# Optimization experiments

Measured on AMD Instinct MI355X. Metric: run time of the kernel, lower is better.

## Reference

```python
import jax, jax.numpy as jnp
import numpy as np

D = 64        # GatedGraphConv out_channels
N_LAYERS = 5  # number of stacked convs


def setup_inputs() -> dict:
    key = jax.random.key(0)
    ks = jax.random.split(key, 16)
    N, E, G = 100000, 1600000, 64
    s = 0.1
    inp = {
        'conv_weight': jax.random.normal(ks[0], (N_LAYERS, D, D), jnp.float32) * s,
        'gru_w_ih':    jax.random.normal(ks[1], (N_LAYERS, 3 * D, D), jnp.float32) * s,
        'gru_w_hh':    jax.random.normal(ks[2], (N_LAYERS, 3 * D, D), jnp.float32) * s,
        'gru_b_ih':    jax.random.normal(ks[3], (N_LAYERS, 3 * D), jnp.float32) * s,
        'gru_b_hh':    jax.random.normal(ks[4], (N_LAYERS, 3 * D), jnp.float32) * s,
        'fc1_w': jax.random.normal(ks[5], (32, D), jnp.float32) * s,
        'fc1_b': jax.random.normal(ks[6], (32,), jnp.float32) * s,
        'fc2_w': jax.random.normal(ks[7], (16, 32), jnp.float32) * s,
        'fc2_b': jax.random.normal(ks[8], (16,), jnp.float32) * s,
        'fc3_w': jax.random.normal(ks[9], (1, 16), jnp.float32) * s,
        'fc3_b': jax.random.normal(ks[10], (1,), jnp.float32) * s,
        'edge_index': jax.random.randint(ks[11], (2, E), 0, N, jnp.int64 if jax.config.jax_enable_x64 else jnp.int32),
        'batch': jnp.sort(jax.random.randint(ks[12], (N,), 0, G, jnp.int32)),
        'num_nodes': N,
        'num_graphs': G,
    }
    return inp


def _gru_cell(m, h, w_ih, w_hh, b_ih, b_hh):
    # torch.nn.GRUCell math; m: [N,D] input, h: [N,D] hidden
    gi = m @ w_ih.T + b_ih   # [N, 3D]
    gh = h @ w_hh.T + b_hh   # [N, 3D]
    i_r, i_z, i_n = jnp.split(gi, 3, axis=1)
    h_r, h_z, h_n = jnp.split(gh, 3, axis=1)
    r = jax.nn.sigmoid(i_r + h_r)
    z = jax.nn.sigmoid(i_z + h_z)
    n = jnp.tanh(i_n + r * h_n)
    return (1.0 - z) * n + z * h


def reference(conv_weight, gru_w_ih, gru_w_hh, gru_b_ih, gru_b_hh,
              fc1_w, fc1_b, fc2_w, fc2_b, fc3_w, fc3_b,
              edge_index, batch, num_nodes, num_graphs):
    src, dst = edge_index[0], edge_index[1]  # source_to_target flow
    # initial node features: zeros [N,8] zero-padded to D by GatedGraphConv
    x0 = jnp.zeros((num_nodes, D), jnp.float32)

    def step(x, params):
        w, wih, whh, bih, bhh = params
        m = x @ w                                        # [N, D]
        agg = jax.ops.segment_sum(m[src], dst, num_segments=num_nodes)  # scatter-add
        return _gru_cell(agg, x, wih, whh, bih, bhh), None

    x, _ = jax.lax.scan(step, x0,
                        (conv_weight, gru_w_ih, gru_w_hh, gru_b_ih, gru_b_hh))

    # scatter_add pooling over batch -> [num_graphs, D]
    g = jax.ops.segment_sum(x, batch, num_segments=num_graphs)
    h = jax.nn.elu(g @ fc1_w.T + fc1_b)
    h = jax.nn.elu(h @ fc2_w.T + fc2_b)
    return h @ fc3_w.T + fc3_b  # [num_graphs, 1]
```

## Files before the change

### kernel.cpp

```cpp
#include <hip/hip_runtime.h>
#include <math.h>

typedef _Float16 f16x2 __attribute__((ext_vector_type(2)));
typedef _Float16 f16x4 __attribute__((ext_vector_type(4)));
typedef _Float16 f16x8 __attribute__((ext_vector_type(8)));
typedef float f32x4 __attribute__((ext_vector_type(4)));

#define CBITS 10
#define FCHUNK 4096
#define MATSZ 13056
__device__ __forceinline__ int woff(int row) { return 64 * row + 8 * (row >> 1); }

__device__ __forceinline__ float sigmoidf_(float v) {
  return 1.0f / (1.0f + __expf(-v));
}
__device__ __forceinline__ float tanhf_(float v) {
  v = fminf(fmaxf(v, -15.f), 15.f);
  float e = __expf(2.f * v);
  return (e - 1.f) / (e + 1.f);
}
__device__ __forceinline__ float eluf_(float v) { return v > 0.f ? v : (__expf(v) - 1.f); }

__global__ __launch_bounds__(256) void fuse_w_kernel(const float* __restrict__ conv_w,
                                                     const float* __restrict__ w_ih,
                                                     _Float16* __restrict__ wcS) {
  const int l = blockIdx.x >> 2;
  const int j0 = (blockIdx.x & 3) * 48;
  const float* W = conv_w + (size_t)l * 4096;
  const float* wi = w_ih + (size_t)l * 12288;
  _Float16* out = wcS + (size_t)l * MATSZ;
  __shared__ float sWt[64 * 68];
  __shared__ float sI[48 * 64];
  const int t = threadIdx.x;
  for (int i = t; i < 4096; i += 256) sWt[(i & 63) * 68 + (i >> 6)] = W[i];
  for (int i = t; i < 3072; i += 256) sI[i] = wi[j0 * 64 + i];
  __syncthreads();
#pragma unroll
  for (int r = 0; r < 3; ++r) {
    int u = t + 256 * r;
    int j = u >> 4, cg = (u & 15) * 4;
    float4 a = {0.f, 0.f, 0.f, 0.f};
    for (int k = 0; k < 64; ++k) {
      float4 w = *(const float4*)(sWt + k * 68 + cg);
      float s = sI[j * 64 + k];
      a.x += w.x * s; a.y += w.y * s; a.z += w.z * s; a.w += w.w * s;
    }
    int row = j0 + j;
    f16x4 hv;
    hv[0] = (_Float16)a.x; hv[1] = (_Float16)a.y;
    hv[2] = (_Float16)a.z; hv[3] = (_Float16)a.w;
    *(f16x4*)(out + woff(row) + cg) = hv;
  }
}

__global__ __launch_bounds__(256) void whh_prep_kernel(const float* __restrict__ whh,
                                                       _Float16* __restrict__ whhS) {
  int idx = blockIdx.x * 256 + threadIdx.x;
  if (idx >= 15360) return;
  int l = idx / 3072, rem = idx % 3072;
  int r = rem >> 4, c4 = (rem & 15) * 4;
  float4 v = *(const float4*)(whh + (size_t)l * 12288 + r * 64 + c4);
  f16x4 hv;
  hv[0] = (_Float16)v.x; hv[1] = (_Float16)v.y;
  hv[2] = (_Float16)v.z; hv[3] = (_Float16)v.w;
  *(f16x4*)(whhS + (size_t)l * MATSZ + woff(r) + c4) = hv;
}

__global__ __launch_bounds__(256) void bucket_hist_kernel(const int* __restrict__ dst,
                                                          int* __restrict__ bh, int E) {
  __shared__ int h[128];
  const int t = threadIdx.x;
  if (t < 128) h[t] = 0;
  __syncthreads();
  for (int e = blockIdx.x * 256 + t; e < E; e += gridDim.x * 256)
    atomicAdd(&h[dst[e] >> CBITS], 1);
  __syncthreads();
  if (t < 128 && h[t]) atomicAdd(&bh[t * 16], h[t]);
}

__global__ __launch_bounds__(128) void bucket_scan_kernel(int* __restrict__ bh, int nbk,
                                                          int* __restrict__ boffs, int E) {
  __shared__ int s[128];
  const int t = threadIdx.x;
  int v = (t < nbk) ? bh[t * 16] : 0;
  s[t] = v;
  __syncthreads();
  for (int o = 1; o < 128; o <<= 1) {
    int a = (t >= o) ? s[t - o] : 0;
    __syncthreads();
    s[t] += a;
    __syncthreads();
  }
  if (t < nbk) {
    int ex = s[t] - v;
    boffs[t] = ex;
    bh[t * 16] = ex;
  }
  if (t == 0) boffs[nbk] = E;
}

__global__ __launch_bounds__(256) void bucket_fill_kernel(const int* __restrict__ src,
                                                          const int* __restrict__ dst,
                                                          int* __restrict__ bcur,
                                                          unsigned* __restrict__ pairs, int E) {
  __shared__ uint2 staged[FCHUNK];
  __shared__ int h[128], lbase[128], gbase[128], lcur[128];
  const int t = threadIdx.x;
  const int e0 = blockIdx.x * FCHUNK;
  int cnt = E - e0;
  if (cnt > FCHUNK) cnt = FCHUNK;
  if (t < 128) h[t] = 0;
  __syncthreads();
  for (int i = t; i < cnt; i += 256) atomicAdd(&h[dst[e0 + i] >> CBITS], 1);
  __syncthreads();
  if (t < 128) lcur[t] = h[t];
  __syncthreads();
  for (int o = 1; o < 128; o <<= 1) {
    int a = 0;
    if (t < 128 && t >= o) a = lcur[t - o];
    __syncthreads();
    if (t < 128) lcur[t] += a;
    __syncthreads();
  }
  if (t < 128) {
    int ex = lcur[t] - h[t];
    lbase[t] = ex;
    if (h[t]) gbase[t] = atomicAdd(&bcur[t * 16], h[t]);
    lcur[t] = ex;
  }
  __syncthreads();
  for (int i = t; i < cnt; i += 256) {
    int d = dst[e0 + i];
    int b = d >> CBITS;
    int p = atomicAdd(&lcur[b], 1);
    staged[p] = make_uint2((unsigned)src[e0 + i], (unsigned)d);
  }
  __syncthreads();
  for (int i = t; i < cnt; i += 256) {
    uint2 pr = staged[i];
    int b = (int)(pr.y >> CBITS);
    pairs[gbase[b] + (i - lbase[b])] = (pr.x << CBITS) | (pr.y & ((1u << CBITS) - 1));
  }
}

__global__ __launch_bounds__(256) void csr_build_kernel(const unsigned* __restrict__ pairs,
                                                        const int* __restrict__ boffs,
                                                        int* __restrict__ offs,
                                                        int* __restrict__ srcs, int N, int E) {
  const int b = blockIdx.x, t = threadIdx.x;
  const int nbase = b << CBITS;
  __shared__ int deg[1024];
  __shared__ int ssc[256];
  for (int i = t; i < 1024; i += 256) deg[i] = 0;
  __syncthreads();
  const int beg = boffs[b], end = boffs[b + 1];
  for (int e = beg + t; e < end; e += 256) atomicAdd(&deg[pairs[e] & 1023], 1);
  __syncthreads();
  int d0 = deg[4 * t], d1 = deg[4 * t + 1], d2 = deg[4 * t + 2], d3 = deg[4 * t + 3];
  int s = d0 + d1 + d2 + d3;
  ssc[t] = s;
  __syncthreads();
  for (int o = 1; o < 256; o <<= 1) {
    int a = (t >= o) ? ssc[t - o] : 0;
    __syncthreads();
    ssc[t] += a;
    __syncthreads();
  }
  int base = beg + ssc[t] - s;
  int c0 = base, c1 = c0 + d0, c2 = c1 + d1, c3 = c2 + d2;
  if (nbase + 4 * t + 0 < N) offs[nbase + 4 * t + 0] = c0;
  if (nbase + 4 * t + 1 < N) offs[nbase + 4 * t + 1] = c1;
  if (nbase + 4 * t + 2 < N) offs[nbase + 4 * t + 2] = c2;
  if (nbase + 4 * t + 3 < N) offs[nbase + 4 * t + 3] = c3;
  deg[4 * t] = c0; deg[4 * t + 1] = c1; deg[4 * t + 2] = c2; deg[4 * t + 3] = c3;
  if (b == 0 && t == 0) offs[N] = E;
  if (b == 0 && t < 64) srcs[E + t] = 0;
  __syncthreads();
  for (int e = beg + t; e < end; e += 256) {
    unsigned p = pairs[e];
    int pos = atomicAdd(&deg[p & 1023], 1);
    srcs[pos] = (int)(p >> CBITS);
  }
}

__global__ __launch_bounds__(64) void h1_kernel(const float* __restrict__ b_ih,
                                                const float* __restrict__ b_hh,
                                                float* __restrict__ h1) {
  int d = threadIdx.x;
  float r = sigmoidf_(b_ih[d] + b_hh[d]);
  float z = sigmoidf_(b_ih[64 + d] + b_hh[64 + d]);
  float n = tanhf_(b_ih[128 + d] + r * b_hh[128 + d]);
  h1[d] = (1.f - z) * n;
}

__global__ __launch_bounds__(256) void bcast_kernel(const int* __restrict__ offs,
                                                    const float* __restrict__ h1,
                                                    _Float16* __restrict__ xh,
                                                    _Float16* __restrict__ aggh,
                                                    int N, int units) {
  int idx = blockIdx.x * 256 + threadIdx.x;
  if (idx >= units) return;
  int v = idx >> 5, lp = idx & 31;
  float2 hh = *(const float2*)(h1 + lp * 2);
  f16x2 hv;
  hv[0] = (_Float16)hh.x; hv[1] = (_Float16)hh.y;
  *(f16x2*)(xh + (size_t)idx * 2) = hv;
  float dg = (v < N) ? (float)(offs[v + 1] - offs[v]) : 0.f;
  f16x2 av;
  av[0] = (_Float16)(dg * hh.x); av[1] = (_Float16)(dg * hh.y);
  *(f16x2*)(aggh + (size_t)idx * 2) = av;
}

__global__ __launch_bounds__(256) void agg_kernel(const _Float16* __restrict__ xh,
                                                  const int* __restrict__ offs,
                                                  const int* __restrict__ srcs,
                                                  _Float16* __restrict__ aggh, int N) {
  int wave = threadIdx.x >> 6, lane = threadIdx.x & 63;
  int v = blockIdx.x * 4 + wave;
  if (v >= N) return;
  const int beg = offs[v], end = offs[v + 1];
  const int deg = end - beg;
  const int og = lane >> 3;
  const int lp = lane & 7;
  f16x8 acc = {};
  for (int base = 0; base < deg; base += 64) {
    const int cnt = min(64, deg - base);
    int sidx = srcs[beg + base + lane];
    for (int e = 0; e < cnt; e += 8) {
      int me = e + og;
      int s = __shfl(sidx, me);
      f16x8 vv = *(const f16x8*)(xh + (size_t)s * 64 + lp * 8);
      if (me < cnt) acc += vv;
    }
  }
#pragma unroll
  for (int off = 8; off < 64; off <<= 1) {
    union { f16x8 h; int i[4]; } a, b;
    a.h = acc;
#pragma unroll
    for (int w = 0; w < 4; ++w) b.i[w] = __shfl_xor(a.i[w], off);
    acc += b.h;
  }
  if (og == 0) *(f16x8*)(aggh + (size_t)v * 64 + lp * 8) = acc;
}

__global__ __launch_bounds__(256) void gru_kernel(const _Float16* __restrict__ aggh,
                                                  _Float16* __restrict__ xh,
                                                  const _Float16* __restrict__ wcS,
                                                  const _Float16* __restrict__ whhS,
                                                  const float* __restrict__ b_ih,
                                                  const float* __restrict__ b_hh,
                                                  int N, int numTiles) {
  __shared__ _Float16 sW[2 * MATSZ];
  const int t = threadIdx.x;
  for (int i = t; i < 2 * (MATSZ / 8); i += 256) {
    int mat = (i >= MATSZ / 8);
    int idx = i - mat * (MATSZ / 8);
    *(f16x8*)(sW + mat * MATSZ + idx * 8) =
        *(const f16x8*)((mat ? whhS : wcS) + idx * 8);
  }
  __syncthreads();
  const int wave = t >> 6, lane = t & 63;
  const int q = lane >> 4, c = lane & 15;
  float bRZ[4], bZZ[4], bIN[4], bHN[4];
#pragma unroll
  for (int dt = 0; dt < 4; ++dt) {
    int d = dt * 16 + c;
    bRZ[dt] = b_ih[d] + b_hh[d];
    bZZ[dt] = b_ih[64 + d] + b_hh[64 + d];
    bIN[dt] = b_ih[128 + d];
    bHN[dt] = b_hh[128 + d];
  }
  f16x8 idf[4];
#pragma unroll
  for (int dt = 0; dt < 4; ++dt) {
    int tgt = (dt & 1) * 16 + c - q * 8;
#pragma unroll
    for (int j = 0; j < 8; ++j) idf[dt][j] = (j == tgt) ? (_Float16)1.0f : (_Float16)0.0f;
  }
  for (int tile = blockIdx.x; tile < numTiles; tile += gridDim.x) {
    const int nb0 = tile * 64 + wave * 16;
    const size_t rowbase = (size_t)(nb0 + c) * 64;
    f16x8 aA[2], aH[2];
#pragma unroll
    for (int ks = 0; ks < 2; ++ks) {
      aA[ks] = *(const f16x8*)(aggh + rowbase + ks * 32 + q * 8);
      aH[ks] = *(const f16x8*)(xh + rowbase + ks * 32 + q * 8);
    }
    f32x4 aR[4], aZ[4], aN[4], aHNa[4], aHO[4];
#pragma unroll
    for (int dt = 0; dt < 4; ++dt) {
      aR[dt] = (f32x4){bRZ[dt], bRZ[dt], bRZ[dt], bRZ[dt]};
      aZ[dt] = (f32x4){bZZ[dt], bZZ[dt], bZZ[dt], bZZ[dt]};
      aN[dt] = (f32x4){bIN[dt], bIN[dt], bIN[dt], bIN[dt]};
      aHNa[dt] = (f32x4){bHN[dt], bHN[dt], bHN[dt], bHN[dt]};
      aHO[dt] = (f32x4){0.f, 0.f, 0.f, 0.f};
    }
#pragma unroll
    for (int ks = 0; ks < 2; ++ks) {
      const int colo = ks * 32 + q * 8;
#pragma unroll
      for (int dt = 0; dt < 4; ++dt) {
        const int r0 = dt * 16 + c;
        f16x8 bWr = *(const f16x8*)(sW + woff(r0) + colo);
        f16x8 bHr = *(const f16x8*)(sW + MATSZ + woff(r0) + colo);
        f16x8 bWz = *(const f16x8*)(sW + woff(64 + r0) + colo);
        f16x8 bHz = *(const f16x8*)(sW + MATSZ + woff(64 + r0) + colo);
        f16x8 bWn = *(const f16x8*)(sW + woff(128 + r0) + colo);
        f16x8 bHn = *(const f16x8*)(sW + MATSZ + woff(128 + r0) + colo);
        aR[dt] = __builtin_amdgcn_mfma_f32_16x16x32_f16(aA[ks], bWr, aR[dt], 0, 0, 0);
        aR[dt] = __builtin_amdgcn_mfma_f32_16x16x32_f16(aH[ks], bHr, aR[dt], 0, 0, 0);
        aZ[dt] = __builtin_amdgcn_mfma_f32_16x16x32_f16(aA[ks], bWz, aZ[dt], 0, 0, 0);
        aZ[dt] = __builtin_amdgcn_mfma_f32_16x16x32_f16(aH[ks], bHz, aZ[dt], 0, 0, 0);
        aN[dt] = __builtin_amdgcn_mfma_f32_16x16x32_f16(aA[ks], bWn, aN[dt], 0, 0, 0);
        aHNa[dt] = __builtin_amdgcn_mfma_f32_16x16x32_f16(aH[ks], bHn, aHNa[dt], 0, 0, 0);
      }
    }
#pragma unroll
    for (int dt = 0; dt < 4; ++dt)
      aHO[dt] = __builtin_amdgcn_mfma_f32_16x16x32_f16(aH[dt >> 1], idf[dt], aHO[dt], 0, 0, 0);
#pragma unroll
    for (int dt = 0; dt < 4; ++dt) {
      int d = dt * 16 + c;
#pragma unroll
      for (int r = 0; r < 4; ++r) {
        int node = nb0 + q * 4 + r;
        if (node < N) {
          float rr = sigmoidf_(aR[dt][r]);
          float zz = sigmoidf_(aZ[dt][r]);
          float nn = tanhf_(aN[dt][r] + rr * aHNa[dt][r]);
          float out = nn + zz * (aHO[dt][r] - nn);
          xh[(size_t)node * 64 + d] = (_Float16)out;
        }
      }
    }
  }
}

__global__ __launch_bounds__(256) void pool_kernel(const _Float16* __restrict__ xh,
                                                   const int* __restrict__ batch,
                                                   float* __restrict__ g, int N) {
  int wave = threadIdx.x >> 6, lane = threadIdx.x & 63;
  int n0 = blockIdx.x * 64 + wave * 16;
  if (n0 >= N) return;
  int end = n0 + 16;
  if (end > N) end = N;
  int cur = batch[n0];
  float acc = 0.f;
  for (int n = n0; n < end; ++n) {
    int b = batch[n];
    if (b != cur) {
      atomicAdd(&g[(size_t)cur * 64 + lane], acc);
      acc = 0.f;
      cur = b;
    }
    acc += (float)xh[(size_t)n * 64 + lane];
  }
  atomicAdd(&g[(size_t)cur * 64 + lane], acc);
}

__global__ __launch_bounds__(256) void mlp_kernel(const float* __restrict__ g,
                                                  const float* __restrict__ w1,
                                                  const float* __restrict__ b1,
                                                  const float* __restrict__ w2,
                                                  const float* __restrict__ b2,
                                                  const float* __restrict__ w3,
                                                  const float* __restrict__ b3,
                                                  float* __restrict__ out, int G) {
  __shared__ float sG[64 * 64];
  __shared__ float sH1[64 * 32];
  __shared__ float sH2[64 * 16];
  int t = threadIdx.x;
  for (int i = t; i < G * 64; i += 256) sG[i] = g[i];
  __syncthreads();
  for (int o = t; o < G * 32; o += 256) {
    int gi = o >> 5, i = o & 31;
    float a = b1[i];
    for (int k = 0; k < 64; ++k) a += sG[gi * 64 + k] * w1[i * 64 + k];
    sH1[gi * 32 + i] = eluf_(a);
  }
  __syncthreads();
  for (int o = t; o < G * 16; o += 256) {
    int gi = o >> 4, i = o & 15;
    float a = b2[i];
    for (int k = 0; k < 32; ++k) a += sH1[gi * 32 + k] * w2[i * 32 + k];
    sH2[gi * 16 + i] = eluf_(a);
  }
  __syncthreads();
  for (int o = t; o < G; o += 256) {
    float a = b3[0];
    for (int k = 0; k < 16; ++k) a += sH2[o * 16 + k] * w3[k];
    out[o] = a;
  }
}

extern "C" void kernel_launch(void* const* d_in, const int* in_sizes, int n_in,
                              void* d_out, int out_size, void* d_ws, size_t ws_size,
                              hipStream_t stream) {
  const float* conv_w = (const float*)d_in[0];
  const float* w_ih = (const float*)d_in[1];
  const float* w_hh = (const float*)d_in[2];
  const float* b_ih = (const float*)d_in[3];
  const float* b_hh = (const float*)d_in[4];
  const float* fc1_w = (const float*)d_in[5];
  const float* fc1_b = (const float*)d_in[6];
  const float* fc2_w = (const float*)d_in[7];
  const float* fc2_b = (const float*)d_in[8];
  const float* fc3_w = (const float*)d_in[9];
  const float* fc3_b = (const float*)d_in[10];
  const int* ei = (const int*)d_in[11];
  const int* batch = (const int*)d_in[12];
  const int N = in_sizes[12];
  const int E = in_sizes[11] / 2;
  const int G = out_size;
  const int* src = ei;
  const int* dst = ei + E;
  const int nbk = (N + 1023) >> CBITS;
  const int tiles = (N + 63) / 64;
  const int Npad = tiles * 64;

  char* ws = (char*)d_ws;
  size_t off = 0;
  auto alloc = [&](size_t bytes) -> void* {
    void* p = ws + off;
    off += (bytes + 255) & ~(size_t)255;
    return p;
  };
  _Float16* xh = (_Float16*)alloc((size_t)Npad * 64 * 2);
  _Float16* aggh = (_Float16*)alloc((size_t)Npad * 64 * 2);
  _Float16* wcS = (_Float16*)alloc((size_t)5 * MATSZ * 2);
  _Float16* whhS = (_Float16*)alloc((size_t)5 * MATSZ * 2);
  float* h1 = (float*)alloc(64 * 4);
  float* gbuf = (float*)alloc((size_t)G * 64 * 4);
  int* offs = (int*)alloc((size_t)(N + 1) * 4);
  int* srcs = (int*)alloc((size_t)(E + 64) * 4);
  unsigned* pairs = (unsigned*)alloc((size_t)E * 4);
  int* bh = (int*)alloc(128 * 16 * 4);
  int* boffs = (int*)alloc(129 * 4);

  hipMemsetAsync(bh, 0, 128 * 16 * 4, stream);
  bucket_hist_kernel<<<256, 256, 0, stream>>>(dst, bh, E);
  bucket_scan_kernel<<<1, 128, 0, stream>>>(bh, nbk, boffs, E);
  bucket_fill_kernel<<<(E + FCHUNK - 1) / FCHUNK, 256, 0, stream>>>(src, dst, bh, pairs, E);
  csr_build_kernel<<<nbk, 256, 0, stream>>>(pairs, boffs, offs, srcs, N, E);

  fuse_w_kernel<<<20, 256, 0, stream>>>(conv_w, w_ih, wcS);
  whh_prep_kernel<<<60, 256, 0, stream>>>(w_hh, whhS);

  h1_kernel<<<1, 64, 0, stream>>>(b_ih, b_hh, h1);
  bcast_kernel<<<(Npad * 32 + 255) / 256, 256, 0, stream>>>(offs, h1, xh, aggh, N, Npad * 32);

  gru_kernel<<<768, 256, 0, stream>>>(aggh, xh, wcS + MATSZ, whhS + MATSZ,
                                      b_ih + 192, b_hh + 192, N, tiles);
  for (int l = 2; l < 5; ++l) {
    agg_kernel<<<(N + 3) / 4, 256, 0, stream>>>(xh, offs, srcs, aggh, N);
    gru_kernel<<<768, 256, 0, stream>>>(aggh, xh, wcS + (size_t)l * MATSZ,
                                        whhS + (size_t)l * MATSZ, b_ih + (size_t)l * 192,
                                        b_hh + (size_t)l * 192, N, tiles);
  }

  hipMemsetAsync(gbuf, 0, (size_t)G * 64 * 4, stream);
  pool_kernel<<<(N + 63) / 64, 256, 0, stream>>>(xh, batch, gbuf, N);
  mlp_kernel<<<1, 256, 0, stream>>>(gbuf, fc1_w, fc1_b, fc2_w, fc2_b, fc3_w, fc3_b,
                                    (float*)d_out, G);
}
```

Before: 448.0 us.

## Split GRU tiles into output-column halves with ping-pong hidden-state buffers

Each GRU work item now computes only half of the 64 output columns for a 64-node tile, which doubles the number of work items and halves the accumulator registers per wave. This should raise occupancy and spread the work across more parallel units. Because two work items now read the same node rows while writing different columns, the hidden state becomes double-buffered (separate input and output arrays) so an in-place write cannot corrupt another item's read. The cost is that the aggregated-message and hidden-state rows are loaded twice, and one extra buffer is allocated.

```diff
diff --git a/kernel.cpp b/kernel.cpp
--- a/kernel.cpp
+++ b/kernel.cpp
@@ -245,12 +245,13 @@
 }
 
 __global__ __launch_bounds__(256) void gru_kernel(const _Float16* __restrict__ aggh,
-                                                  _Float16* __restrict__ xh,
+                                                  const _Float16* __restrict__ xh_in,
+                                                  _Float16* __restrict__ xh_out,
                                                   const _Float16* __restrict__ wcS,
                                                   const _Float16* __restrict__ whhS,
                                                   const float* __restrict__ b_ih,
                                                   const float* __restrict__ b_hh,
-                                                  int N, int numTiles) {
+                                                  int N, int numIter) {
   __shared__ _Float16 sW[2 * MATSZ];
   const int t = threadIdx.x;
   for (int i = t; i < 2 * (MATSZ / 8); i += 256) {
@@ -271,66 +272,72 @@
     bIN[dt] = b_ih[128 + d];
     bHN[dt] = b_hh[128 + d];
   }
-  f16x8 idf[4];
-#pragma unroll
-  for (int dt = 0; dt < 4; ++dt) {
-    int tgt = (dt & 1) * 16 + c - q * 8;
-#pragma unroll
-    for (int j = 0; j < 8; ++j) idf[dt][j] = (j == tgt) ? (_Float16)1.0f : (_Float16)0.0f;
-  }
-  for (int tile = blockIdx.x; tile < numTiles; tile += gridDim.x) {
+  f16x8 idf[2];
+#pragma unroll
+  for (int p = 0; p < 2; ++p) {
+    int tgt = p * 16 + c - q * 8;
+#pragma unroll
+    for (int j = 0; j < 8; ++j) idf[p][j] = (j == tgt) ? (_Float16)1.0f : (_Float16)0.0f;
+  }
+#pragma unroll 1
+  for (int it = blockIdx.x; it < numIter; it += gridDim.x) {
+    const int tile = it >> 1, half = it & 1;
     const int nb0 = tile * 64 + wave * 16;
     const size_t rowbase = (size_t)(nb0 + c) * 64;
     f16x8 aA[2], aH[2];
 #pragma unroll
     for (int ks = 0; ks < 2; ++ks) {
       aA[ks] = *(const f16x8*)(aggh + rowbase + ks * 32 + q * 8);
-      aH[ks] = *(const f16x8*)(xh + rowbase + ks * 32 + q * 8);
-    }
-    f32x4 aR[4], aZ[4], aN[4], aHNa[4], aHO[4];
-#pragma unroll
-    for (int dt = 0; dt < 4; ++dt) {
-      aR[dt] = (f32x4){bRZ[dt], bRZ[dt], bRZ[dt], bRZ[dt]};
-      aZ[dt] = (f32x4){bZZ[dt], bZZ[dt], bZZ[dt], bZZ[dt]};
-      aN[dt] = (f32x4){bIN[dt], bIN[dt], bIN[dt], bIN[dt]};
-      aHNa[dt] = (f32x4){bHN[dt], bHN[dt], bHN[dt], bHN[dt]};
-      aHO[dt] = (f32x4){0.f, 0.f, 0.f, 0.f};
+      aH[ks] = *(const f16x8*)(xh_in + rowbase + ks * 32 + q * 8);
+    }
+    f32x4 aR[2], aZ[2], aN[2], aHNa[2], aHO[2];
+#pragma unroll
+    for (int p = 0; p < 2; ++p) {
+      float brz = half ? bRZ[2 + p] : bRZ[p];
+      float bzz = half ? bZZ[2 + p] : bZZ[p];
+      float bin = half ? bIN[2 + p] : bIN[p];
+      float bhn = half ? bHN[2 + p] : bHN[p];
+      aR[p] = (f32x4){brz, brz, brz, brz};
+      aZ[p] = (f32x4){bzz, bzz, bzz, bzz};
+      aN[p] = (f32x4){bin, bin, bin, bin};
+      aHNa[p] = (f32x4){bhn, bhn, bhn, bhn};
+      aHO[p] = (f32x4){0.f, 0.f, 0.f, 0.f};
     }
 #pragma unroll
     for (int ks = 0; ks < 2; ++ks) {
       const int colo = ks * 32 + q * 8;
 #pragma unroll
-      for (int dt = 0; dt < 4; ++dt) {
-        const int r0 = dt * 16 + c;
+      for (int p = 0; p < 2; ++p) {
+        const int r0 = (half * 2 + p) * 16 + c;
         f16x8 bWr = *(const f16x8*)(sW + woff(r0) + colo);
         f16x8 bHr = *(const f16x8*)(sW + MATSZ + woff(r0) + colo);
         f16x8 bWz = *(const f16x8*)(sW + woff(64 + r0) + colo);
         f16x8 bHz = *(const f16x8*)(sW + MATSZ + woff(64 + r0) + colo);
         f16x8 bWn = *(const f16x8*)(sW + woff(128 + r0) + colo);
         f16x8 bHn = *(const f16x8*)(sW + MATSZ + woff(128 + r0) + colo);
-        aR[dt] = __builtin_amdgcn_mfma_f32_16x16x32_f16(aA[ks], bWr, aR[dt], 0, 0, 0);
-        aR[dt] = __builtin_amdgcn_mfma_f32_16x16x32_f16(aH[ks], bHr, aR[dt], 0, 0, 0);
-        aZ[dt] = __builtin_amdgcn_mfma_f32_16x16x32_f16(aA[ks], bWz, aZ[dt], 0, 0, 0);
-        aZ[dt] = __builtin_amdgcn_mfma_f32_16x16x32_f16(aH[ks], bHz, aZ[dt], 0, 0, 0);
-        aN[dt] = __builtin_amdgcn_mfma_f32_16x16x32_f16(aA[ks], bWn, aN[dt], 0, 0, 0);
-        aHNa[dt] = __builtin_amdgcn_mfma_f32_16x16x32_f16(aH[ks], bHn, aHNa[dt], 0, 0, 0);
+        aR[p] = __builtin_amdgcn_mfma_f32_16x16x32_f16(aA[ks], bWr, aR[p], 0, 0, 0);
+        aR[p] = __builtin_amdgcn_mfma_f32_16x16x32_f16(aH[ks], bHr, aR[p], 0, 0, 0);
+        aZ[p] = __builtin_amdgcn_mfma_f32_16x16x32_f16(aA[ks], bWz, aZ[p], 0, 0, 0);
+        aZ[p] = __builtin_amdgcn_mfma_f32_16x16x32_f16(aH[ks], bHz, aZ[p], 0, 0, 0);
+        aN[p] = __builtin_amdgcn_mfma_f32_16x16x32_f16(aA[ks], bWn, aN[p], 0, 0, 0);
+        aHNa[p] = __builtin_amdgcn_mfma_f32_16x16x32_f16(aH[ks], bHn, aHNa[p], 0, 0, 0);
       }
     }
 #pragma unroll
-    for (int dt = 0; dt < 4; ++dt)
-      aHO[dt] = __builtin_amdgcn_mfma_f32_16x16x32_f16(aH[dt >> 1], idf[dt], aHO[dt], 0, 0, 0);
-#pragma unroll
-    for (int dt = 0; dt < 4; ++dt) {
-      int d = dt * 16 + c;
+    for (int p = 0; p < 2; ++p)
+      aHO[p] = __builtin_amdgcn_mfma_f32_16x16x32_f16(aH[half], idf[p], aHO[p], 0, 0, 0);
+#pragma unroll
+    for (int p = 0; p < 2; ++p) {
+      int d = (half * 2 + p) * 16 + c;
 #pragma unroll
       for (int r = 0; r < 4; ++r) {
         int node = nb0 + q * 4 + r;
         if (node < N) {
-          float rr = sigmoidf_(aR[dt][r]);
-          float zz = sigmoidf_(aZ[dt][r]);
-          float nn = tanhf_(aN[dt][r] + rr * aHNa[dt][r]);
-          float out = nn + zz * (aHO[dt][r] - nn);
-          xh[(size_t)node * 64 + d] = (_Float16)out;
+          float rr = sigmoidf_(aR[p][r]);
+          float zz = sigmoidf_(aZ[p][r]);
+          float nn = tanhf_(aN[p][r] + rr * aHNa[p][r]);
+          float out = nn + zz * (aHO[p][r] - nn);
+          xh_out[(size_t)node * 64 + d] = (_Float16)out;
         }
       }
     }
@@ -418,6 +425,7 @@
   const int nbk = (N + 1023) >> CBITS;
   const int tiles = (N + 63) / 64;
   const int Npad = tiles * 64;
+  const int gruIter = tiles * 2;
 
   char* ws = (char*)d_ws;
   size_t off = 0;
@@ -426,7 +434,8 @@
     off += (bytes + 255) & ~(size_t)255;
     return p;
   };
-  _Float16* xh = (_Float16*)alloc((size_t)Npad * 64 * 2);
+  _Float16* xhA = (_Float16*)alloc((size_t)Npad * 64 * 2);
+  _Float16* xhB = (_Float16*)alloc((size_t)Npad * 64 * 2);
   _Float16* aggh = (_Float16*)alloc((size_t)Npad * 64 * 2);
   _Float16* wcS = (_Float16*)alloc((size_t)5 * MATSZ * 2);
   _Float16* whhS = (_Float16*)alloc((size_t)5 * MATSZ * 2);
@@ -448,19 +457,23 @@
   whh_prep_kernel<<<60, 256, 0, stream>>>(w_hh, whhS);
 
   h1_kernel<<<1, 64, 0, stream>>>(b_ih, b_hh, h1);
-  bcast_kernel<<<(Npad * 32 + 255) / 256, 256, 0, stream>>>(offs, h1, xh, aggh, N, Npad * 32);
-
-  gru_kernel<<<768, 256, 0, stream>>>(aggh, xh, wcS + MATSZ, whhS + MATSZ,
-                                      b_ih + 192, b_hh + 192, N, tiles);
+  bcast_kernel<<<(Npad * 32 + 255) / 256, 256, 0, stream>>>(offs, h1, xhA, aggh, N, Npad * 32);
+
+  _Float16* cur = xhA;
+  _Float16* nxt = xhB;
+  gru_kernel<<<768, 256, 0, stream>>>(aggh, cur, nxt, wcS + MATSZ, whhS + MATSZ,
+                                      b_ih + 192, b_hh + 192, N, gruIter);
+  { _Float16* tmp = cur; cur = nxt; nxt = tmp; }
   for (int l = 2; l < 5; ++l) {
-    agg_kernel<<<(N + 3) / 4, 256, 0, stream>>>(xh, offs, srcs, aggh, N);
-    gru_kernel<<<768, 256, 0, stream>>>(aggh, xh, wcS + (size_t)l * MATSZ,
+    agg_kernel<<<(N + 3) / 4, 256, 0, stream>>>(cur, offs, srcs, aggh, N);
+    gru_kernel<<<768, 256, 0, stream>>>(aggh, cur, nxt, wcS + (size_t)l * MATSZ,
                                         whhS + (size_t)l * MATSZ, b_ih + (size_t)l * 192,
-                                        b_hh + (size_t)l * 192, N, tiles);
+                                        b_hh + (size_t)l * 192, N, gruIter);
+    _Float16* tmp = cur; cur = nxt; nxt = tmp;
   }
 
   hipMemsetAsync(gbuf, 0, (size_t)G * 64 * 4, stream);
-  pool_kernel<<<(N + 63) / 64, 256, 0, stream>>>(xh, batch, gbuf, N);
+  pool_kernel<<<(N + 63) / 64, 256, 0, stream>>>(cur, batch, gbuf, N);
   mlp_kernel<<<1, 256, 0, stream>>>(gbuf, fc1_w, fc1_b, fc2_w, fc2_b, fc3_w, fc3_b,
                                     (float*)d_out, G);
 }
```

Result: faster. 423.4 us (-5.5%).
